# Performance work log

Hardware: AMD Instinct MI355X
Metric: run time of the kernel (lower is better)

The kernel has to match this reference:

```python
import jax, jax.numpy as jnp
import numpy as np

N_NODES = 50000
N_EDGES = 800000
IN_F = 128
OUT_F = 32
HEADS = 4
EDGE_F = 32  # must equal OUT_F for the original module's shapes to broadcast


def setup_inputs() -> dict:
    key = jax.random.key(0)
    k1, k2, k3, k4, k5, k6, k7 = jax.random.split(key, 7)
    h = jax.random.normal(k1, (N_NODES, IN_F), dtype=jnp.float32)
    edge_indices = jax.random.randint(k2, (2, N_EDGES), 0, N_NODES, dtype=jnp.int32)
    edge_attr = jax.random.normal(k3, (N_EDGES, EDGE_F), dtype=jnp.float32)
    # learned parameters (xavier-ish scaling)
    W = jax.random.normal(k4, (IN_F, HEADS * OUT_F), dtype=jnp.float32) * (1.0 / np.sqrt(IN_F))
    a = jax.random.normal(k5, (HEADS, 2 * OUT_F + EDGE_F), dtype=jnp.float32) * 0.1
    eW = jax.random.normal(k6, (EDGE_F, HEADS * OUT_F), dtype=jnp.float32) * (1.0 / np.sqrt(EDGE_F))
    eb = jnp.zeros((HEADS * OUT_F,), dtype=jnp.float32)
    return {"h": h, "edge_indices": edge_indices, "edge_attr": edge_attr,
            "W": W, "a": a, "eW": eW, "eb": eb}


def reference(h, edge_indices, edge_attr, W, a, eW, eb):
    N = h.shape[0]
    H = a.shape[0]
    F = W.shape[1] // H
    row, col = edge_indices[0], edge_indices[1]

    # node / edge projections
    ht = (h @ W).reshape(N, H, F)                       # [N,H,F]
    et = (edge_attr @ eW + eb).reshape(-1, H, F)        # [E,H,F]

    # split attention vector; avoids materializing the [E,H,3F] concat
    a_i, a_j, a_e = a[:, :F], a[:, F:2 * F], a[:, 2 * F:]
    alpha_i = jnp.einsum('nhf,hf->nh', ht, a_i)         # [N,H]
    alpha_j = jnp.einsum('nhf,hf->nh', ht, a_j)         # [N,H]
    e = alpha_i[row] + alpha_j[col] + jnp.einsum('ehf,hf->eh', et, a_e)  # [E,H]
    e = jax.nn.leaky_relu(e, negative_slope=0.2)

    # scatter-softmax over edges grouped by destination (row), global-max stabilized
    e_exp = jnp.exp(e - jnp.max(e))                     # matches torch exp(e - e.max())
    denom = jax.ops.segment_sum(e_exp, row, num_segments=N)  # [N,H]
    att = e_exp / (denom[row] + 1e-8)                   # [E,H]

    # weighted scatter-add aggregation
    hj = ht[col]                                        # [E,H,F]
    h_out = jax.ops.segment_sum(att[:, :, None] * hj, row, num_segments=N)  # [N,H,F]
    h_out = h_out.reshape(N, H * F)                     # concat=True
    h_out = jax.nn.elu(h_out)                           # dropout=0 (eval)
    return h_out, att
```

## Files before the change

### kernel.cpp

```cpp
#include <hip/hip_runtime.h>
#include <hip/hip_bf16.h>
#include <hip/hip_fp16.h>

#define N_NODES 50000
#define N_EDGES 800000
#define IN_F 128
#define OUT_F 32
#define HEADS 4
#define EDGE_F 32
#define HF 128
#define SB 256
#define NBLK ((N_NODES + SB - 1) / SB)

typedef __attribute__((ext_vector_type(8))) short short8_t;
typedef __attribute__((ext_vector_type(4))) float f32x4;

__device__ __forceinline__ unsigned short f2bf(float x) {
    unsigned int u = __float_as_uint(x);
    unsigned int r = (u + 0x7FFF + ((u >> 16) & 1)) >> 16;
    return (unsigned short)r;
}
__device__ __forceinline__ float bf2f(unsigned short b) {
    return __uint_as_float(((unsigned int)b) << 16);
}

__global__ void prep_kernel(const float* __restrict__ eW, const float* __restrict__ eb,
                            const float* __restrict__ a,
                            float* __restrict__ w_eff, float* __restrict__ b_eff) {
    int t = threadIdx.x;
    if (t < 128) {
        int k = t >> 2, h = t & 3;
        float s = 0.f;
        #pragma unroll
        for (int f = 0; f < EDGE_F; ++f)
            s = fmaf(eW[k * HF + h * OUT_F + f], a[h * 96 + 2 * OUT_F + f], s);
        w_eff[k * 4 + h] = s;
    } else if (t < 132) {
        int h = t - 128;
        float s = 0.f;
        #pragma unroll
        for (int f = 0; f < EDGE_F; ++f)
            s = fmaf(eb[h * OUT_F + f], a[h * 96 + 2 * OUT_F + f], s);
        b_eff[h] = s;
    }
}

__global__ __launch_bounds__(256) void prepW_kernel(const float* __restrict__ W,
                                                    unsigned short* __restrict__ W_T) {
    int g = blockIdx.x * 256 + threadIdx.x;
    int n = g >> 4, c = g & 15;
    unsigned short w8[8];
    #pragma unroll
    for (int q = 0; q < 8; ++q)
        w8[q] = f2bf(W[(size_t)(8 * c + q) * 128 + n]);
    *(uint4*)&W_T[n * 128 + ((c ^ (n & 7)) << 3)] = *(uint4*)w8;
}

__global__ __launch_bounds__(256) void node_kernel(
        const float* __restrict__ h, const unsigned short* __restrict__ W_T,
        const float* __restrict__ a,
        __hip_bfloat16* __restrict__ ht_bf,
        float* __restrict__ alpha_i, float* __restrict__ alpha_j) {
    __shared__ __align__(16) unsigned short Wl[128 * 128];
    __shared__ __align__(16) unsigned short Hhi[64 * 128];
    __shared__ __align__(16) unsigned short Hlo[64 * 128];
    int t = threadIdx.x;
    int lane = t & 63, wave = t >> 6;
    int nb = blockIdx.x * 64;
    {
        const uint4* src = (const uint4*)W_T;
        uint4* dst = (uint4*)Wl;
        #pragma unroll
        for (int u = 0; u < 8; ++u) dst[t + u * 256] = src[t + u * 256];
    }
    #pragma unroll
    for (int u = 0; u < 8; ++u) {
        int f = u * 256 + t;
        int row = f >> 5, q = f & 31;
        int gn = nb + row; if (gn > N_NODES - 1) gn = N_NODES - 1;
        float4 v = ((const float4*)h)[(size_t)gn * 32 + q];
        unsigned short hi[4], lo[4];
        #pragma unroll
        for (int x = 0; x < 4; ++x) {
            float xv = (&v.x)[x];
            unsigned short hb = f2bf(xv);
            hi[x] = hb;
            lo[x] = f2bf(xv - bf2f(hb));
        }
        int c = q >> 1, half = q & 1;
        int off = row * 128 + ((c ^ (row & 7)) << 3) + half * 4;
        *(uint2*)&Hhi[off] = *(uint2*)hi;
        *(uint2*)&Hlo[off] = *(uint2*)lo;
    }
    __syncthreads();
    int n0 = nb + wave * 16;
    if (n0 >= N_NODES) return;
    int r = lane & 15, g = lane >> 4;
    short8_t ahi[4], alo[4];
    #pragma unroll
    for (int k = 0; k < 4; ++k) {
        int c = k * 4 + g;
        int off = (wave * 16 + r) * 128 + ((c ^ (r & 7)) << 3);
        ahi[k] = *(const short8_t*)&Hhi[off];
        alo[k] = *(const short8_t*)&Hlo[off];
    }
    f32x4 acc[8];
    #pragma unroll
    for (int i = 0; i < 8; ++i) acc[i] = (f32x4){0.f, 0.f, 0.f, 0.f};
    #pragma unroll
    for (int tt = 0; tt < 8; ++tt) {
        int n = tt * 16 + r;
        #pragma unroll
        for (int k = 0; k < 4; ++k) {
            int c = k * 4 + g;
            short8_t b = *(const short8_t*)&Wl[n * 128 + ((c ^ (n & 7)) << 3)];
            acc[tt] = __builtin_amdgcn_mfma_f32_16x16x32_bf16(ahi[k], b, acc[tt], 0, 0, 0);
            acc[tt] = __builtin_amdgcn_mfma_f32_16x16x32_bf16(alo[k], b, acc[tt], 0, 0, 0);
        }
    }
    #pragma unroll
    for (int tt = 0; tt < 8; ++tt)
        #pragma unroll
        for (int reg = 0; reg < 4; ++reg) {
            int rowg = n0 + 4 * g + reg;
            ((unsigned short*)ht_bf)[(size_t)rowg * 128 + tt * 16 + r] = f2bf(acc[tt][reg]);
        }
    float pi[4][4], pj[4][4];
    #pragma unroll
    for (int hh = 0; hh < 4; ++hh) {
        float ai0 = a[hh * 96 + r],      ai1 = a[hh * 96 + 16 + r];
        float aj0 = a[hh * 96 + 32 + r], aj1 = a[hh * 96 + 48 + r];
        #pragma unroll
        for (int reg = 0; reg < 4; ++reg) {
            float v0 = acc[2 * hh][reg], v1 = acc[2 * hh + 1][reg];
            pi[hh][reg] = fmaf(v0, ai0, v1 * ai1);
            pj[hh][reg] = fmaf(v0, aj0, v1 * aj1);
        }
    }
    #pragma unroll
    for (int hh = 0; hh < 4; ++hh)
        #pragma unroll
        for (int reg = 0; reg < 4; ++reg) {
            float vi = pi[hh][reg], vj = pj[hh][reg];
            #pragma unroll
            for (int s = 1; s < 16; s <<= 1) {
                vi += __shfl_xor(vi, s, 64);
                vj += __shfl_xor(vj, s, 64);
            }
            pi[hh][reg] = vi; pj[hh][reg] = vj;
        }
    if (r == 0) {
        #pragma unroll
        for (int hh = 0; hh < 4; ++hh)
            #pragma unroll
            for (int reg = 0; reg < 4; ++reg) {
                int rowg = n0 + 4 * g + reg;
                alpha_i[rowg * 4 + hh] = pi[hh][reg];
                alpha_j[rowg * 4 + hh] = pj[hh][reg];
            }
    }
}

__global__ __launch_bounds__(256) void count_kernel(const int* __restrict__ row,
                                                    int* __restrict__ deg,
                                                    int* __restrict__ rank) {
    int t = blockIdx.x * 256 + threadIdx.x;
    if (t < N_EDGES / 4) {
        int4 r4 = ((const int4*)row)[t];
        int4 k4;
        k4.x = atomicAdd(&deg[r4.x], 1);
        k4.y = atomicAdd(&deg[r4.y], 1);
        k4.z = atomicAdd(&deg[r4.z], 1);
        k4.w = atomicAdd(&deg[r4.w], 1);
        ((int4*)rank)[t] = k4;
    }
}

__device__ __forceinline__ int block_incl_scan(int v, int lane, int wid, int* wsum) {
    int x = v;
    #pragma unroll
    for (int s = 1; s < 64; s <<= 1) {
        int y = __shfl_up(x, s, 64);
        if (lane >= s) x += y;
    }
    if (lane == 63) wsum[wid] = x;
    __syncthreads();
    int add = 0;
    #pragma unroll
    for (int w = 0; w < 4; ++w) add += (w < wid) ? wsum[w] : 0;
    return x + add;
}

__global__ __launch_bounds__(SB) void scan1_kernel(const int* __restrict__ deg,
                                                   int* __restrict__ row_off,
                                                   int* __restrict__ blk_sums) {
    __shared__ int wsum[4];
    int i = blockIdx.x * SB + threadIdx.x;
    int v = (i < N_NODES) ? deg[i] : 0;
    int incl = block_incl_scan(v, threadIdx.x & 63, threadIdx.x >> 6, wsum);
    if (i < N_NODES) row_off[i] = incl - v;
    if (threadIdx.x == SB - 1) blk_sums[blockIdx.x] = incl;
}

__global__ __launch_bounds__(SB) void scan2_kernel(int* __restrict__ blk_sums,
                                                   int* __restrict__ blk_off,
                                                   int* __restrict__ row_off) {
    __shared__ int wsum[4];
    int t = threadIdx.x;
    int v = (t < NBLK) ? blk_sums[t] : 0;
    int incl = block_incl_scan(v, t & 63, t >> 6, wsum);
    if (t < NBLK) blk_off[t] = incl - v;
    if (t == SB - 1) row_off[N_NODES] = incl;
}

__global__ __launch_bounds__(SB) void scan3_kernel(const int* __restrict__ blk_off,
                                                   int* __restrict__ row_off) {
    int i = blockIdx.x * SB + threadIdx.x;
    if (i < N_NODES)
        row_off[i] += blk_off[blockIdx.x];
}

__global__ __launch_bounds__(256) void edge_kernel(
        const int* __restrict__ row, const int* __restrict__ col,
        const float* __restrict__ ea,
        const float* __restrict__ w_eff, const float* __restrict__ b_eff,
        const float* __restrict__ alpha_i, const float* __restrict__ alpha_j,
        const int* __restrict__ row_off, const int* __restrict__ rank,
        uint4* __restrict__ rec, float* __restrict__ att_ex) {
    __shared__ __align__(16) float eas[256 * 36];
    __shared__ float wsd[128];
    __shared__ float bs[4];
    int t = threadIdx.x;
    if (t < 128) wsd[t] = w_eff[t];
    if (t < 4) bs[t] = b_eff[t];
    int e0 = blockIdx.x * 256;
    {
        const float4* src = (const float4*)ea + (size_t)e0 * 8;
        #pragma unroll
        for (int u = 0; u < 8; ++u) {
            int f = u * 256 + t;
            int el = f >> 3, j = f & 7;
            *(float4*)&eas[el * 36 + 4 * j] = src[f];
        }
    }
    __syncthreads();
    int e = e0 + t;
    float4 ev[8];
    #pragma unroll
    for (int i = 0; i < 8; ++i) ev[i] = *(const float4*)&eas[t * 36 + 4 * i];
    int r = row[e], c = col[e];
    int rk = rank[e];
    float4 ai = *(const float4*)(alpha_i + (size_t)r * 4);
    float4 aj = *(const float4*)(alpha_j + (size_t)c * 4);
    float s0 = bs[0], s1 = bs[1], s2 = bs[2], s3 = bs[3];
    #pragma unroll
    for (int i = 0; i < 8; ++i) {
        #pragma unroll
        for (int kk = 0; kk < 4; ++kk) {
            float x = (&ev[i].x)[kk];
            float4 w4 = *(const float4*)&wsd[(i * 4 + kk) * 4];
            s0 = fmaf(x, w4.x, s0);
            s1 = fmaf(x, w4.y, s1);
            s2 = fmaf(x, w4.z, s2);
            s3 = fmaf(x, w4.w, s3);
        }
    }
    float e0v = s0 + ai.x + aj.x;
    float e1v = s1 + ai.y + aj.y;
    float e2v = s2 + ai.z + aj.z;
    float e3v = s3 + ai.w + aj.w;
    e0v = e0v > 0.f ? e0v : 0.2f * e0v;
    e1v = e1v > 0.f ? e1v : 0.2f * e1v;
    e2v = e2v > 0.f ? e2v : 0.2f * e2v;
    e3v = e3v > 0.f ? e3v : 0.2f * e3v;
    float x0 = __expf(e0v), x1 = __expf(e1v), x2 = __expf(e2v), x3 = __expf(e3v);
    ((float4*)att_ex)[e] = make_float4(x0, x1, x2, x3);
    __half2 p01 = __floats2half2_rn(x0, x1);
    __half2 p23 = __floats2half2_rn(x2, x3);
    uint4 out;
    out.x = *reinterpret_cast<unsigned int*>(&p01);
    out.y = *reinterpret_cast<unsigned int*>(&p23);
    out.z = (unsigned int)c;
    out.w = 0u;
    int pos = row_off[r] + rk;
    rec[pos] = out;
}

__global__ __launch_bounds__(256) void agg_kernel(
        const int* __restrict__ row_off, const uint4* __restrict__ rec,
        const __hip_bfloat16* __restrict__ ht_bf,
        float* __restrict__ hout, float* __restrict__ rden_buf) {
    int wave = threadIdx.x >> 6;
    int lane = threadIdx.x & 63;
    int n = blockIdx.x * 4 + wave;
    if (n >= N_NODES) return;
    int beg = row_off[n], end = row_off[n + 1];
    int h2 = lane >> 4;
    int sh = (h2 & 1) * 16;
    float2 acc0 = {0.f, 0.f}, acc1 = {0.f, 0.f};
    float den0 = 0.f, den1 = 0.f;
    int p = beg;
    for (; p + 3 < end; p += 4) {
        uint4 rA = rec[p];
        uint4 rB = rec[p + 1];
        uint4 rC = rec[p + 2];
        uint4 rD = rec[p + 3];
        unsigned int wA = (h2 & 2) ? rA.y : rA.x;
        unsigned int wB = (h2 & 2) ? rB.y : rB.x;
        unsigned int wC = (h2 & 2) ? rC.y : rC.x;
        unsigned int wD = (h2 & 2) ? rD.y : rD.x;
        float exA = __half2float(__ushort_as_half((unsigned short)(wA >> sh)));
        float exB = __half2float(__ushort_as_half((unsigned short)(wB >> sh)));
        float exC = __half2float(__ushort_as_half((unsigned short)(wC >> sh)));
        float exD = __half2float(__ushort_as_half((unsigned short)(wD >> sh)));
        float2 hvA = __bfloat1622float2(
            *(const __hip_bfloat162*)(ht_bf + (size_t)rA.z * HF + 2 * lane));
        float2 hvB = __bfloat1622float2(
            *(const __hip_bfloat162*)(ht_bf + (size_t)rB.z * HF + 2 * lane));
        float2 hvC = __bfloat1622float2(
            *(const __hip_bfloat162*)(ht_bf + (size_t)rC.z * HF + 2 * lane));
        float2 hvD = __bfloat1622float2(
            *(const __hip_bfloat162*)(ht_bf + (size_t)rD.z * HF + 2 * lane));
        acc0.x = fmaf(exA, hvA.x, acc0.x); acc0.y = fmaf(exA, hvA.y, acc0.y);
        acc1.x = fmaf(exB, hvB.x, acc1.x); acc1.y = fmaf(exB, hvB.y, acc1.y);
        acc0.x = fmaf(exC, hvC.x, acc0.x); acc0.y = fmaf(exC, hvC.y, acc0.y);
        acc1.x = fmaf(exD, hvD.x, acc1.x); acc1.y = fmaf(exD, hvD.y, acc1.y);
        den0 += exA + exC; den1 += exB + exD;
    }
    for (; p < end; ++p) {
        uint4 rA = rec[p];
        unsigned int wA = (h2 & 2) ? rA.y : rA.x;
        float exA = __half2float(__ushort_as_half((unsigned short)(wA >> sh)));
        float2 hvA = __bfloat1622float2(
            *(const __hip_bfloat162*)(ht_bf + (size_t)rA.z * HF + 2 * lane));
        acc0.x = fmaf(exA, hvA.x, acc0.x); acc0.y = fmaf(exA, hvA.y, acc0.y);
        den0 += exA;
    }
    float den = den0 + den1;
    float rden = 1.0f / (den + 1e-8f);
    float ox = (acc0.x + acc1.x) * rden, oy = (acc0.y + acc1.y) * rden;
    ox = ox > 0.f ? ox : expm1f(ox);
    oy = oy > 0.f ? oy : expm1f(oy);
    float2 o = {ox, oy};
    ((float2*)(hout + (size_t)n * HF))[lane] = o;
    if ((lane & 15) == 0)
        rden_buf[n * 4 + h2] = rden;
}

__global__ __launch_bounds__(256) void norm_kernel(const int* __restrict__ row,
                                                   const float* __restrict__ rden_buf,
                                                   float* __restrict__ att) {
    int e = blockIdx.x * 256 + threadIdx.x;
    float4 ex = ((const float4*)att)[e];
    int r = row[e];
    float4 rd = *(const float4*)(rden_buf + (size_t)r * 4);
    ex.x *= rd.x; ex.y *= rd.y; ex.z *= rd.z; ex.w *= rd.w;
    ((float4*)att)[e] = ex;
}

extern "C" void kernel_launch(void* const* d_in, const int* in_sizes, int n_in,
                              void* d_out, int out_size, void* d_ws, size_t ws_size,
                              hipStream_t stream) {
    const float* h  = (const float*)d_in[0];
    const int*   ei = (const int*)  d_in[1];
    const float* ea = (const float*)d_in[2];
    const float* W  = (const float*)d_in[3];
    const float* a  = (const float*)d_in[4];
    const float* eW = (const float*)d_in[5];
    const float* eb = (const float*)d_in[6];

    float* out  = (float*)d_out;
    float* hout = out;
    float* att  = out + (size_t)N_NODES * HF;

    char* wsb = (char*)d_ws;
    __hip_bfloat16* ht_bf = (__hip_bfloat16*)wsb;
    float* alpha_i = (float*)(wsb + (size_t)N_NODES * HF * 2);
    float* alpha_j = alpha_i + N_NODES * HEADS;
    float* w_eff   = alpha_j + N_NODES * HEADS;
    float* b_eff   = w_eff + 128;
    unsigned short* W_T = (unsigned short*)(b_eff + 4);
    int*   deg     = (int*)(W_T + 128 * 128);
    int*   row_off = deg + N_NODES;
    int*   blk_sums= row_off + N_NODES + 1;
    int*   blk_off = blk_sums + NBLK;
    int*   rank    = (int*)((((uintptr_t)(blk_off + NBLK)) + 15) & ~(uintptr_t)15);
    uint4* rec     = (uint4*)((((uintptr_t)(rank + N_EDGES)) + 15) & ~(uintptr_t)15);
    float* rden_buf= (float*)(rec + N_EDGES);

    const int* row = ei;
    const int* col = ei + N_EDGES;

    hipMemsetAsync(deg, 0, (size_t)N_NODES * sizeof(int), stream);

    prep_kernel<<<1, 160, 0, stream>>>(eW, eb, a, w_eff, b_eff);
    prepW_kernel<<<8, 256, 0, stream>>>(W, W_T);
    node_kernel<<<(N_NODES + 63) / 64, 256, 0, stream>>>(h, W_T, a, ht_bf, alpha_i, alpha_j);
    count_kernel<<<(N_EDGES / 4 + 255) / 256, 256, 0, stream>>>(row, deg, rank);
    scan1_kernel<<<NBLK, SB, 0, stream>>>(deg, row_off, blk_sums);
    scan2_kernel<<<1, SB, 0, stream>>>(blk_sums, blk_off, row_off);
    scan3_kernel<<<NBLK, SB, 0, stream>>>(blk_off, row_off);
    edge_kernel<<<N_EDGES / 256, 256, 0, stream>>>(row, col, ea, w_eff, b_eff,
                                                   alpha_i, alpha_j, row_off, rank,
                                                   rec, att);
    agg_kernel<<<(N_NODES + 3) / 4, 256, 0, stream>>>(row_off, rec, ht_bf, hout, rden_buf);
    norm_kernel<<<N_EDGES / 256, 256, 0, stream>>>(row, rden_buf, att);
}
```

Before: 328.2 us.

## Split edge kernel into projection and scatter passes with packed node records

The fused edge kernel is split in two. proj_kernel computes the per-edge attention projection from edge_attr and writes it out. edge_scatter then handles four edges per thread with vectorized row/col/rank loads, and builds each CSR record using nontemporal stores. scan3 now also packs alpha_i and the row offset into one 32-byte per-node record, so the row-side gather touches a single cache line. In exchange, the projection results make an extra round trip through memory and there is one more kernel launch.

Result: slower. 351.5 us (+7.1%).

```diff
diff --git a/kernel.cpp b/kernel.cpp
--- a/kernel.cpp
+++ b/kernel.cpp
@@ -14,6 +14,7 @@
 
 typedef __attribute__((ext_vector_type(8))) short short8_t;
 typedef __attribute__((ext_vector_type(4))) float f32x4;
+typedef __attribute__((ext_vector_type(4))) unsigned int u32x4;
 
 __device__ __forceinline__ unsigned short f2bf(float x) {
     unsigned int u = __float_as_uint(x);
@@ -214,19 +215,25 @@
 }
 
 __global__ __launch_bounds__(SB) void scan3_kernel(const int* __restrict__ blk_off,
-                                                   int* __restrict__ row_off) {
+                                                   int* __restrict__ row_off,
+                                                   const float* __restrict__ alpha_i,
+                                                   float4* __restrict__ nrec) {
     int i = blockIdx.x * SB + threadIdx.x;
-    if (i < N_NODES)
-        row_off[i] += blk_off[blockIdx.x];
-}
-
-__global__ __launch_bounds__(256) void edge_kernel(
-        const int* __restrict__ row, const int* __restrict__ col,
+    if (i < N_NODES) {
+        int v = row_off[i] + blk_off[blockIdx.x];
+        row_off[i] = v;
+        float4 ai = *(const float4*)(alpha_i + (size_t)i * 4);
+        nrec[(size_t)i * 2] = ai;
+        float4 m;
+        m.x = __int_as_float(v); m.y = 0.f; m.z = 0.f; m.w = 0.f;
+        nrec[(size_t)i * 2 + 1] = m;
+    }
+}
+
+__global__ __launch_bounds__(256) void proj_kernel(
         const float* __restrict__ ea,
         const float* __restrict__ w_eff, const float* __restrict__ b_eff,
-        const float* __restrict__ alpha_i, const float* __restrict__ alpha_j,
-        const int* __restrict__ row_off, const int* __restrict__ rank,
-        uint4* __restrict__ rec, float* __restrict__ att_ex) {
+        float4* __restrict__ proj) {
     __shared__ __align__(16) float eas[256 * 36];
     __shared__ float wsd[128];
     __shared__ float bs[4];
@@ -248,10 +255,6 @@
     float4 ev[8];
     #pragma unroll
     for (int i = 0; i < 8; ++i) ev[i] = *(const float4*)&eas[t * 36 + 4 * i];
-    int r = row[e], c = col[e];
-    int rk = rank[e];
-    float4 ai = *(const float4*)(alpha_i + (size_t)r * 4);
-    float4 aj = *(const float4*)(alpha_j + (size_t)c * 4);
     float s0 = bs[0], s1 = bs[1], s2 = bs[2], s3 = bs[3];
     #pragma unroll
     for (int i = 0; i < 8; ++i) {
@@ -265,25 +268,56 @@
             s3 = fmaf(x, w4.w, s3);
         }
     }
-    float e0v = s0 + ai.x + aj.x;
-    float e1v = s1 + ai.y + aj.y;
-    float e2v = s2 + ai.z + aj.z;
-    float e3v = s3 + ai.w + aj.w;
-    e0v = e0v > 0.f ? e0v : 0.2f * e0v;
-    e1v = e1v > 0.f ? e1v : 0.2f * e1v;
-    e2v = e2v > 0.f ? e2v : 0.2f * e2v;
-    e3v = e3v > 0.f ? e3v : 0.2f * e3v;
-    float x0 = __expf(e0v), x1 = __expf(e1v), x2 = __expf(e2v), x3 = __expf(e3v);
-    ((float4*)att_ex)[e] = make_float4(x0, x1, x2, x3);
-    __half2 p01 = __floats2half2_rn(x0, x1);
-    __half2 p23 = __floats2half2_rn(x2, x3);
-    uint4 out;
-    out.x = *reinterpret_cast<unsigned int*>(&p01);
-    out.y = *reinterpret_cast<unsigned int*>(&p23);
-    out.z = (unsigned int)c;
-    out.w = 0u;
-    int pos = row_off[r] + rk;
-    rec[pos] = out;
+    proj[e] = make_float4(s0, s1, s2, s3);
+}
+
+__global__ __launch_bounds__(256) void edge_scatter(
+        const int* __restrict__ row, const int* __restrict__ col,
+        const int* __restrict__ rank,
+        const float4* __restrict__ proj, const float4* __restrict__ nrec,
+        const float* __restrict__ alpha_j,
+        uint4* __restrict__ rec, float4* __restrict__ att_ex) {
+    int t = blockIdx.x * 256 + threadIdx.x;
+    if (t >= N_EDGES / 4) return;
+    int4 r4 = ((const int4*)row)[t];
+    int4 c4 = ((const int4*)col)[t];
+    int4 k4 = ((const int4*)rank)[t];
+    int rr[4] = {r4.x, r4.y, r4.z, r4.w};
+    int cc[4] = {c4.x, c4.y, c4.z, c4.w};
+    int kk[4] = {k4.x, k4.y, k4.z, k4.w};
+    float4 p[4];
+    #pragma unroll
+    for (int i = 0; i < 4; ++i) p[i] = proj[4 * t + i];
+    float4 ai[4], aj[4];
+    int ro[4];
+    #pragma unroll
+    for (int i = 0; i < 4; ++i) {
+        ai[i] = nrec[(size_t)rr[i] * 2];
+        ro[i] = ((const int*)nrec)[(size_t)rr[i] * 8 + 4];
+        aj[i] = *(const float4*)(alpha_j + (size_t)cc[i] * 4);
+    }
+    #pragma unroll
+    for (int i = 0; i < 4; ++i) {
+        float e0v = p[i].x + ai[i].x + aj[i].x;
+        float e1v = p[i].y + ai[i].y + aj[i].y;
+        float e2v = p[i].z + ai[i].z + aj[i].z;
+        float e3v = p[i].w + ai[i].w + aj[i].w;
+        e0v = e0v > 0.f ? e0v : 0.2f * e0v;
+        e1v = e1v > 0.f ? e1v : 0.2f * e1v;
+        e2v = e2v > 0.f ? e2v : 0.2f * e2v;
+        e3v = e3v > 0.f ? e3v : 0.2f * e3v;
+        float x0 = __expf(e0v), x1 = __expf(e1v), x2 = __expf(e2v), x3 = __expf(e3v);
+        att_ex[4 * t + i] = make_float4(x0, x1, x2, x3);
+        __half2 p01 = __floats2half2_rn(x0, x1);
+        __half2 p23 = __floats2half2_rn(x2, x3);
+        u32x4 o;
+        o.x = *reinterpret_cast<unsigned int*>(&p01);
+        o.y = *reinterpret_cast<unsigned int*>(&p23);
+        o.z = (unsigned int)cc[i];
+        o.w = 0u;
+        int pos = ro[i] + kk[i];
+        __builtin_nontemporal_store(o, (u32x4*)&rec[pos]);
+    }
 }
 
 __global__ __launch_bounds__(256) void agg_kernel(
@@ -387,11 +421,13 @@
     int*   rank    = (int*)((((uintptr_t)(blk_off + NBLK)) + 15) & ~(uintptr_t)15);
     uint4* rec     = (uint4*)((((uintptr_t)(rank + N_EDGES)) + 15) & ~(uintptr_t)15);
     float* rden_buf= (float*)(rec + N_EDGES);
+    float4* nrec   = (float4*)(rden_buf + N_NODES * 4);
+    float4* proj   = nrec + (size_t)N_NODES * 2;
 
     const int* row = ei;
     const int* col = ei + N_EDGES;
 
-    hipMemsetAsync(deg, 0, (size_t)N_NODES * sizeof(int), stream);
+    (void)hipMemsetAsync(deg, 0, (size_t)N_NODES * sizeof(int), stream);
 
     prep_kernel<<<1, 160, 0, stream>>>(eW, eb, a, w_eff, b_eff);
     prepW_kernel<<<8, 256, 0, stream>>>(W, W_T);
@@ -399,10 +435,10 @@
     count_kernel<<<(N_EDGES / 4 + 255) / 256, 256, 0, stream>>>(row, deg, rank);
     scan1_kernel<<<NBLK, SB, 0, stream>>>(deg, row_off, blk_sums);
     scan2_kernel<<<1, SB, 0, stream>>>(blk_sums, blk_off, row_off);
-    scan3_kernel<<<NBLK, SB, 0, stream>>>(blk_off, row_off);
-    edge_kernel<<<N_EDGES / 256, 256, 0, stream>>>(row, col, ea, w_eff, b_eff,
-                                                   alpha_i, alpha_j, row_off, rank,
-                                                   rec, att);
+    scan3_kernel<<<NBLK, SB, 0, stream>>>(blk_off, row_off, alpha_i, nrec);
+    proj_kernel<<<N_EDGES / 256, 256, 0, stream>>>(ea, w_eff, b_eff, proj);
+    edge_scatter<<<(N_EDGES / 4 + 255) / 256, 256, 0, stream>>>(
+        row, col, rank, proj, nrec, alpha_j, rec, (float4*)att);
     agg_kernel<<<(N_NODES + 3) / 4, 256, 0, stream>>>(row_off, rec, ht_bf, hout, rden_buf);
     norm_kernel<<<N_EDGES / 256, 256, 0, stream>>>(row, rden_buf, att);
 }
```

## Pack alpha_i with row offset per node and use nontemporal loads

Applied to the files above, without the earlier changes.

scan3 now writes a per-node 32-byte record holding alpha_i and the final row offset, so edge_kernel fetches both random per-row values from one cache line instead of two separate gathers. edge_kernel drops its LDS staging of edge_attr and instead reads each edge's 128 bytes directly with nontemporal vector loads. agg_kernel also uses nontemporal loads for the streamed edge records. The costs are an extra node-sized buffer, an extra write pass in scan3, and uncoalesced per-thread strided loads of edge_attr in place of the cooperative shared-memory transpose.

New measurement: 367.0 us. +11.8%, slower.

```diff
diff --git a/kernel.cpp b/kernel.cpp
--- a/kernel.cpp
+++ b/kernel.cpp
@@ -14,6 +14,7 @@
 
 typedef __attribute__((ext_vector_type(8))) short short8_t;
 typedef __attribute__((ext_vector_type(4))) float f32x4;
+typedef __attribute__((ext_vector_type(4))) unsigned int u32x4;
 
 __device__ __forceinline__ unsigned short f2bf(float x) {
     unsigned int u = __float_as_uint(x);
@@ -214,50 +215,50 @@
 }
 
 __global__ __launch_bounds__(SB) void scan3_kernel(const int* __restrict__ blk_off,
-                                                   int* __restrict__ row_off) {
+                                                   int* __restrict__ row_off,
+                                                   const float* __restrict__ alpha_i,
+                                                   float4* __restrict__ nrec) {
     int i = blockIdx.x * SB + threadIdx.x;
-    if (i < N_NODES)
-        row_off[i] += blk_off[blockIdx.x];
+    if (i < N_NODES) {
+        int v = row_off[i] + blk_off[blockIdx.x];
+        row_off[i] = v;
+        float4 ai = *(const float4*)(alpha_i + (size_t)i * 4);
+        nrec[(size_t)i * 2] = ai;
+        float4 m;
+        m.x = __int_as_float(v); m.y = 0.f; m.z = 0.f; m.w = 0.f;
+        nrec[(size_t)i * 2 + 1] = m;
+    }
 }
 
 __global__ __launch_bounds__(256) void edge_kernel(
         const int* __restrict__ row, const int* __restrict__ col,
+        const int* __restrict__ rank,
         const float* __restrict__ ea,
         const float* __restrict__ w_eff, const float* __restrict__ b_eff,
-        const float* __restrict__ alpha_i, const float* __restrict__ alpha_j,
-        const int* __restrict__ row_off, const int* __restrict__ rank,
-        uint4* __restrict__ rec, float* __restrict__ att_ex) {
-    __shared__ __align__(16) float eas[256 * 36];
+        const float4* __restrict__ nrec, const float* __restrict__ alpha_j,
+        uint4* __restrict__ rec, float4* __restrict__ att_ex) {
     __shared__ float wsd[128];
     __shared__ float bs[4];
     int t = threadIdx.x;
     if (t < 128) wsd[t] = w_eff[t];
     if (t < 4) bs[t] = b_eff[t];
-    int e0 = blockIdx.x * 256;
-    {
-        const float4* src = (const float4*)ea + (size_t)e0 * 8;
-        #pragma unroll
-        for (int u = 0; u < 8; ++u) {
-            int f = u * 256 + t;
-            int el = f >> 3, j = f & 7;
-            *(float4*)&eas[el * 36 + 4 * j] = src[f];
-        }
-    }
     __syncthreads();
-    int e = e0 + t;
-    float4 ev[8];
-    #pragma unroll
-    for (int i = 0; i < 8; ++i) ev[i] = *(const float4*)&eas[t * 36 + 4 * i];
+    int e = blockIdx.x * 256 + t;
+    const f32x4* src = (const f32x4*)(ea + (size_t)e * EDGE_F);
+    f32x4 ev[8];
+    #pragma unroll
+    for (int i = 0; i < 8; ++i) ev[i] = __builtin_nontemporal_load(src + i);
     int r = row[e], c = col[e];
     int rk = rank[e];
-    float4 ai = *(const float4*)(alpha_i + (size_t)r * 4);
-    float4 aj = *(const float4*)(alpha_j + (size_t)c * 4);
+    f32x4 ai = ((const f32x4*)nrec)[(size_t)r * 2];
+    int ro = ((const int*)nrec)[(size_t)r * 8 + 4];
+    f32x4 aj = *(const f32x4*)(alpha_j + (size_t)c * 4);
     float s0 = bs[0], s1 = bs[1], s2 = bs[2], s3 = bs[3];
     #pragma unroll
     for (int i = 0; i < 8; ++i) {
         #pragma unroll
         for (int kk = 0; kk < 4; ++kk) {
-            float x = (&ev[i].x)[kk];
+            float x = ev[i][kk];
             float4 w4 = *(const float4*)&wsd[(i * 4 + kk) * 4];
             s0 = fmaf(x, w4.x, s0);
             s1 = fmaf(x, w4.y, s1);
@@ -265,25 +266,24 @@
             s3 = fmaf(x, w4.w, s3);
         }
     }
-    float e0v = s0 + ai.x + aj.x;
-    float e1v = s1 + ai.y + aj.y;
-    float e2v = s2 + ai.z + aj.z;
-    float e3v = s3 + ai.w + aj.w;
+    float e0v = s0 + ai[0] + aj[0];
+    float e1v = s1 + ai[1] + aj[1];
+    float e2v = s2 + ai[2] + aj[2];
+    float e3v = s3 + ai[3] + aj[3];
     e0v = e0v > 0.f ? e0v : 0.2f * e0v;
     e1v = e1v > 0.f ? e1v : 0.2f * e1v;
     e2v = e2v > 0.f ? e2v : 0.2f * e2v;
     e3v = e3v > 0.f ? e3v : 0.2f * e3v;
     float x0 = __expf(e0v), x1 = __expf(e1v), x2 = __expf(e2v), x3 = __expf(e3v);
-    ((float4*)att_ex)[e] = make_float4(x0, x1, x2, x3);
+    att_ex[e] = make_float4(x0, x1, x2, x3);
     __half2 p01 = __floats2half2_rn(x0, x1);
     __half2 p23 = __floats2half2_rn(x2, x3);
-    uint4 out;
-    out.x = *reinterpret_cast<unsigned int*>(&p01);
-    out.y = *reinterpret_cast<unsigned int*>(&p23);
-    out.z = (unsigned int)c;
-    out.w = 0u;
-    int pos = row_off[r] + rk;
-    rec[pos] = out;
+    uint4 o;
+    o.x = *reinterpret_cast<unsigned int*>(&p01);
+    o.y = *reinterpret_cast<unsigned int*>(&p23);
+    o.z = (unsigned int)c;
+    o.w = 0u;
+    rec[ro + rk] = o;
 }
 
 __global__ __launch_bounds__(256) void agg_kernel(
@@ -297,30 +297,31 @@
     int beg = row_off[n], end = row_off[n + 1];
     int h2 = lane >> 4;
     int sh = (h2 & 1) * 16;
+    const u32x4* recv = (const u32x4*)rec;
     float2 acc0 = {0.f, 0.f}, acc1 = {0.f, 0.f};
     float den0 = 0.f, den1 = 0.f;
     int p = beg;
     for (; p + 3 < end; p += 4) {
-        uint4 rA = rec[p];
-        uint4 rB = rec[p + 1];
-        uint4 rC = rec[p + 2];
-        uint4 rD = rec[p + 3];
-        unsigned int wA = (h2 & 2) ? rA.y : rA.x;
-        unsigned int wB = (h2 & 2) ? rB.y : rB.x;
-        unsigned int wC = (h2 & 2) ? rC.y : rC.x;
-        unsigned int wD = (h2 & 2) ? rD.y : rD.x;
+        u32x4 rA = __builtin_nontemporal_load(recv + p);
+        u32x4 rB = __builtin_nontemporal_load(recv + p + 1);
+        u32x4 rC = __builtin_nontemporal_load(recv + p + 2);
+        u32x4 rD = __builtin_nontemporal_load(recv + p + 3);
+        unsigned int wA = (h2 & 2) ? rA[1] : rA[0];
+        unsigned int wB = (h2 & 2) ? rB[1] : rB[0];
+        unsigned int wC = (h2 & 2) ? rC[1] : rC[0];
+        unsigned int wD = (h2 & 2) ? rD[1] : rD[0];
         float exA = __half2float(__ushort_as_half((unsigned short)(wA >> sh)));
         float exB = __half2float(__ushort_as_half((unsigned short)(wB >> sh)));
         float exC = __half2float(__ushort_as_half((unsigned short)(wC >> sh)));
         float exD = __half2float(__ushort_as_half((unsigned short)(wD >> sh)));
         float2 hvA = __bfloat1622float2(
-            *(const __hip_bfloat162*)(ht_bf + (size_t)rA.z * HF + 2 * lane));
+            *(const __hip_bfloat162*)(ht_bf + (size_t)rA[2] * HF + 2 * lane));
         float2 hvB = __bfloat1622float2(
-            *(const __hip_bfloat162*)(ht_bf + (size_t)rB.z * HF + 2 * lane));
+            *(const __hip_bfloat162*)(ht_bf + (size_t)rB[2] * HF + 2 * lane));
         float2 hvC = __bfloat1622float2(
-            *(const __hip_bfloat162*)(ht_bf + (size_t)rC.z * HF + 2 * lane));
+            *(const __hip_bfloat162*)(ht_bf + (size_t)rC[2] * HF + 2 * lane));
         float2 hvD = __bfloat1622float2(
-            *(const __hip_bfloat162*)(ht_bf + (size_t)rD.z * HF + 2 * lane));
+            *(const __hip_bfloat162*)(ht_bf + (size_t)rD[2] * HF + 2 * lane));
         acc0.x = fmaf(exA, hvA.x, acc0.x); acc0.y = fmaf(exA, hvA.y, acc0.y);
         acc1.x = fmaf(exB, hvB.x, acc1.x); acc1.y = fmaf(exB, hvB.y, acc1.y);
         acc0.x = fmaf(exC, hvC.x, acc0.x); acc0.y = fmaf(exC, hvC.y, acc0.y);
@@ -328,11 +329,11 @@
         den0 += exA + exC; den1 += exB + exD;
     }
     for (; p < end; ++p) {
-        uint4 rA = rec[p];
-        unsigned int wA = (h2 & 2) ? rA.y : rA.x;
+        u32x4 rA = __builtin_nontemporal_load(recv + p);
+        unsigned int wA = (h2 & 2) ? rA[1] : rA[0];
         float exA = __half2float(__ushort_as_half((unsigned short)(wA >> sh)));
         float2 hvA = __bfloat1622float2(
-            *(const __hip_bfloat162*)(ht_bf + (size_t)rA.z * HF + 2 * lane));
+            *(const __hip_bfloat162*)(ht_bf + (size_t)rA[2] * HF + 2 * lane));
         acc0.x = fmaf(exA, hvA.x, acc0.x); acc0.y = fmaf(exA, hvA.y, acc0.y);
         den0 += exA;
     }
@@ -387,11 +388,12 @@
     int*   rank    = (int*)((((uintptr_t)(blk_off + NBLK)) + 15) & ~(uintptr_t)15);
     uint4* rec     = (uint4*)((((uintptr_t)(rank + N_EDGES)) + 15) & ~(uintptr_t)15);
     float* rden_buf= (float*)(rec + N_EDGES);
+    float4* nrec   = (float4*)(rden_buf + N_NODES * 4);
 
     const int* row = ei;
     const int* col = ei + N_EDGES;
 
-    hipMemsetAsync(deg, 0, (size_t)N_NODES * sizeof(int), stream);
+    (void)hipMemsetAsync(deg, 0, (size_t)N_NODES * sizeof(int), stream);
 
     prep_kernel<<<1, 160, 0, stream>>>(eW, eb, a, w_eff, b_eff);
     prepW_kernel<<<8, 256, 0, stream>>>(W, W_T);
@@ -399,10 +401,9 @@
     count_kernel<<<(N_EDGES / 4 + 255) / 256, 256, 0, stream>>>(row, deg, rank);
     scan1_kernel<<<NBLK, SB, 0, stream>>>(deg, row_off, blk_sums);
     scan2_kernel<<<1, SB, 0, stream>>>(blk_sums, blk_off, row_off);
-    scan3_kernel<<<NBLK, SB, 0, stream>>>(blk_off, row_off);
-    edge_kernel<<<N_EDGES / 256, 256, 0, stream>>>(row, col, ea, w_eff, b_eff,
-                                                   alpha_i, alpha_j, row_off, rank,
-                                                   rec, att);
+    scan3_kernel<<<NBLK, SB, 0, stream>>>(blk_off, row_off, alpha_i, nrec);
+    edge_kernel<<<N_EDGES / 256, 256, 0, stream>>>(row, col, rank, ea, w_eff, b_eff,
+                                                   nrec, alpha_j, rec, (float4*)att);
     agg_kernel<<<(N_NODES + 3) / 4, 256, 0, stream>>>(row_off, rec, ht_bf, hout, rden_buf);
     norm_kernel<<<N_EDGES / 256, 256, 0, stream>>>(row, rden_buf, att);
 }
```
